# Performance work log

Measured on AMD Instinct MI355X. Metric: run time of the kernel, lower is better.

Reference implementation:

```python
import jax, jax.numpy as jnp
import numpy as np

N_NODES = 50000
N_GRAPHS = 128
N_FEATS = 128
HIDDEN = 128
FC_HID = 64
N_CLASSES = 10
N_EDGES = 600000


def gcn_conv(x, W, b, src, dst, n):
    # x: [N, Fin] -> [N, Fout]; symmetric-normalized scatter aggregation (PyG GCNConv)
    h = x @ W  # [N, Fout]
    ones = jnp.ones(src.shape[0], dtype=h.dtype)
    deg = jax.ops.segment_sum(ones, dst, num_segments=n)  # in-degree incl. self loops
    dinv = jnp.where(deg > 0, jax.lax.rsqrt(jnp.maximum(deg, 1.0)), 0.0)
    norm = dinv[src] * dinv[dst]  # [E]
    msg = norm[:, None] * h[src]  # gather + scale, [E, Fout]
    out = jax.ops.segment_sum(msg, dst, num_segments=n)  # scatter-add
    return out + b


def setup_inputs() -> dict:
    key = jax.random.key(0)
    ks = jax.random.split(key, 16)
    x = jax.random.normal(ks[0], (N_NODES, N_FEATS), dtype=jnp.float32)
    edge_index = jax.random.randint(ks[1], (2, N_EDGES), 0, N_NODES, dtype=jnp.int64)
    batch = jnp.sort(jax.random.randint(ks[2], (N_NODES,), 0, N_GRAPHS, dtype=jnp.int64))

    def lin(k, fin, fout):
        s = 1.0 / np.sqrt(fin)
        kw, kb = jax.random.split(k)
        W = jax.random.uniform(kw, (fin, fout), jnp.float32, -s, s)
        b = jax.random.uniform(kb, (fout,), jnp.float32, -s, s)
        return W, b

    W1, b1 = lin(ks[3], N_FEATS, HIDDEN)
    W2, b2 = lin(ks[4], HIDDEN, HIDDEN)
    W3, b3 = lin(ks[5], HIDDEN, HIDDEN)
    Wf1, bf1 = lin(ks[6], HIDDEN, FC_HID)
    Wf2, bf2 = lin(ks[7], FC_HID, N_CLASSES)
    return {"x": x, "edge_index": edge_index, "batch": batch,
            "W1": W1, "b1": b1, "W2": W2, "b2": b2, "W3": W3, "b3": b3,
            "Wf1": Wf1, "bf1": bf1, "Wf2": Wf2, "bf2": bf2}


def reference(x, edge_index, batch, W1, b1, W2, b2, W3, b3, Wf1, bf1, Wf2, bf2):
    n = x.shape[0]
    # add self loops (PyG GCNConv default)
    loop = jnp.arange(n, dtype=edge_index.dtype)
    src = jnp.concatenate([edge_index[0], loop])
    dst = jnp.concatenate([edge_index[1], loop])

    h = jax.nn.relu(gcn_conv(x, W1, b1, src, dst, n))
    h = jax.nn.relu(gcn_conv(h, W2, b2, src, dst, n))
    h = jax.nn.relu(gcn_conv(h, W3, b3, src, dst, n))

    # global mean pool per graph
    sums = jax.ops.segment_sum(h, batch, num_segments=N_GRAPHS)
    cnts = jax.ops.segment_sum(jnp.ones((n,), h.dtype), batch, num_segments=N_GRAPHS)
    hg = sums / jnp.maximum(cnts, 1.0)[:, None]  # [G, HIDDEN]

    h = jax.nn.relu(hg @ Wf1 + bf1)
    return h @ Wf2 + bf2  # [G, N_CLASSES]
```

## Files before the change

### kernel.cpp

```cpp
#include <hip/hip_runtime.h>

#define NFEAT 128
#define NGRAPHS 128
#define FCH 64
#define NCLS 10
#define ELLW 48

__global__ void ell_fill_kernel(const int* __restrict__ src, const int* __restrict__ dst, int E,
                                int* __restrict__ cursor, int* __restrict__ ell) {
    int i = (blockIdx.x * blockDim.x + threadIdx.x) * 4;
    if (i + 3 < E) {
        int4 s4 = *(const int4*)(src + i);
        int4 d4 = *(const int4*)(dst + i);
        int p;
        p = atomicAdd(&cursor[d4.x], 1); if (p < ELLW) ell[(size_t)d4.x * ELLW + p] = s4.x;
        p = atomicAdd(&cursor[d4.y], 1); if (p < ELLW) ell[(size_t)d4.y * ELLW + p] = s4.y;
        p = atomicAdd(&cursor[d4.z], 1); if (p < ELLW) ell[(size_t)d4.z * ELLW + p] = s4.z;
        p = atomicAdd(&cursor[d4.w], 1); if (p < ELLW) ell[(size_t)d4.w * ELLW + p] = s4.w;
    } else {
        for (int j = i; j < E; ++j) {
            int d = dst[j];
            int p = atomicAdd(&cursor[d], 1);
            if (p < ELLW) ell[(size_t)d * ELLW + p] = src[j];
        }
    }
}

__global__ void dinv_kernel(const int* __restrict__ deg, float* __restrict__ dinv, int N) {
    int i = blockIdx.x * blockDim.x + threadIdx.x;
    if (i < N) dinv[i] = rsqrtf((float)(deg[i] + 1));
}

__global__ __launch_bounds__(256)
void gemm128_kernel(const float* __restrict__ X, const float* __restrict__ W,
                    const float* __restrict__ dinv, float* __restrict__ H, int N) {
    __shared__ float4 Ws4[32 * 32];
    int t = threadIdx.x;
    int tx = t & 15;
    int ty = t >> 4;
    int r0 = blockIdx.x * 128 + ty * 8;

    const float* xr[8];
    bool rowok[8];
    #pragma unroll
    for (int i = 0; i < 8; ++i) {
        rowok[i] = (r0 + i < N);
        xr[i] = X + (size_t)(rowok[i] ? (r0 + i) : 0) * NFEAT;
    }

    float acc[8][8];
    #pragma unroll
    for (int i = 0; i < 8; ++i)
        #pragma unroll
        for (int j = 0; j < 8; ++j) acc[i][j] = 0.f;

    const float4* W4 = (const float4*)W;

    for (int ko = 0; ko < 128; ko += 32) {
        #pragma unroll
        for (int i = 0; i < 4; ++i) Ws4[t + i * 256] = W4[ko * 32 + t + i * 256];
        __syncthreads();

        for (int k = 0; k < 32; k += 4) {
            float xk[8][4];
            #pragma unroll
            for (int i = 0; i < 8; ++i) {
                float4 v = *(const float4*)(xr[i] + ko + k);
                xk[i][0] = v.x; xk[i][1] = v.y; xk[i][2] = v.z; xk[i][3] = v.w;
            }
            #pragma unroll
            for (int kk = 0; kk < 4; ++kk) {
                float4 wa = Ws4[(k + kk) * 32 + tx];
                float4 wb = Ws4[(k + kk) * 32 + 16 + tx];
                float w[8] = {wa.x, wa.y, wa.z, wa.w, wb.x, wb.y, wb.z, wb.w};
                #pragma unroll
                for (int i = 0; i < 8; ++i) {
                    float xv = xk[i][kk];
                    #pragma unroll
                    for (int j = 0; j < 8; ++j) acc[i][j] = fmaf(xv, w[j], acc[i][j]);
                }
            }
        }
        __syncthreads();
    }

    #pragma unroll
    for (int i = 0; i < 8; ++i) {
        if (rowok[i]) {
            float di = dinv[r0 + i];
            float* hp = H + (size_t)(r0 + i) * NFEAT;
            float4 o0 = {di * acc[i][0], di * acc[i][1], di * acc[i][2], di * acc[i][3]};
            float4 o1 = {di * acc[i][4], di * acc[i][5], di * acc[i][6], di * acc[i][7]};
            *(float4*)(hp + tx * 4) = o0;
            *(float4*)(hp + 64 + tx * 4) = o1;
        }
    }
}

__global__ __launch_bounds__(256)
void aggregate_kernel(const float* __restrict__ Hs, const int* __restrict__ deg,
                      const int* __restrict__ ell, const float* __restrict__ dinv,
                      const float* __restrict__ bias, float* __restrict__ out, int N) {
    int node = (blockIdx.x * 256 + threadIdx.x) >> 6;
    int lane = threadIdx.x & 63;
    if (node >= N) return;

    int half = lane >> 5;
    int fl = lane & 31;
    const float4* H4 = (const float4*)Hs;

    float di = dinv[node];
    float4 acc = {0.f, 0.f, 0.f, 0.f};
    if (half == 0) acc = H4[(size_t)node * 32 + fl];

    const int* row = ell + (size_t)node * ELLW;
    int d = deg[node]; if (d > ELLW) d = ELLW;
    int e = 0;

    for (; e + 7 < d; e += 8) {
        int s0 = row[e + half], s1 = row[e + 2 + half];
        int s2 = row[e + 4 + half], s3 = row[e + 6 + half];
        float4 v0 = H4[(size_t)s0 * 32 + fl];
        float4 v1 = H4[(size_t)s1 * 32 + fl];
        float4 v2 = H4[(size_t)s2 * 32 + fl];
        float4 v3 = H4[(size_t)s3 * 32 + fl];
        acc.x += v0.x + v1.x + v2.x + v3.x;
        acc.y += v0.y + v1.y + v2.y + v3.y;
        acc.z += v0.z + v1.z + v2.z + v3.z;
        acc.w += v0.w + v1.w + v2.w + v3.w;
    }
    for (; e + 1 < d; e += 2) {
        int s = row[e + half];
        float4 v = H4[(size_t)s * 32 + fl];
        acc.x += v.x; acc.y += v.y; acc.z += v.z; acc.w += v.w;
    }
    if (e < d && half == 0) {
        int s = row[e];
        float4 v = H4[(size_t)s * 32 + fl];
        acc.x += v.x; acc.y += v.y; acc.z += v.z; acc.w += v.w;
    }

    acc.x += __shfl_down(acc.x, 32, 64);
    acc.y += __shfl_down(acc.y, 32, 64);
    acc.z += __shfl_down(acc.z, 32, 64);
    acc.w += __shfl_down(acc.w, 32, 64);

    if (half == 0) {
        float4 b = ((const float4*)bias)[fl];
        float4 o;
        o.x = fmaxf(fmaf(di, acc.x, b.x), 0.f);
        o.y = fmaxf(fmaf(di, acc.y, b.y), 0.f);
        o.z = fmaxf(fmaf(di, acc.z, b.z), 0.f);
        o.w = fmaxf(fmaf(di, acc.w, b.w), 0.f);
        ((float4*)(out + (size_t)node * NFEAT))[fl] = o;
    }
}

__global__ __launch_bounds__(256)
void poolfc_kernel(const float* __restrict__ H, const int* __restrict__ batch, int N,
                   const float* __restrict__ Wf1, const float* __restrict__ bf1,
                   const float* __restrict__ Wf2, const float* __restrict__ bf2,
                   float* __restrict__ out) {
    int g = blockIdx.x;

    int lo = 0, hi = N;
    while (lo < hi) { int mid = (lo + hi) >> 1; if (batch[mid] < g) lo = mid + 1; else hi = mid; }
    int start = lo;
    hi = N;
    while (lo < hi) { int mid = (lo + hi) >> 1; if (batch[mid] < g + 1) lo = mid + 1; else hi = mid; }
    int end = lo;

    int wave = threadIdx.x >> 6;
    int lane = threadIdx.x & 63;

    float2 acc = {0.f, 0.f};
    for (int i = start + wave; i < end; i += 4) {
        float2 v = ((const float2*)(H + (size_t)i * NFEAT))[lane];
        acc.x += v.x; acc.y += v.y;
    }

    __shared__ float2 part[4][64];
    __shared__ float hg[NFEAT];
    __shared__ float h1[FCH];
    part[wave][lane] = acc;
    __syncthreads();

    if (wave == 0) {
        float2 t0 = part[0][lane], t1 = part[1][lane], t2 = part[2][lane], t3 = part[3][lane];
        float c = fmaxf((float)(end - start), 1.0f);
        hg[lane * 2]     = (t0.x + t1.x + t2.x + t3.x) / c;
        hg[lane * 2 + 1] = (t0.y + t1.y + t2.y + t3.y) / c;
        float a = bf1[lane];
        #pragma unroll 4
        for (int k = 0; k < NFEAT; ++k) a = fmaf(hg[k], Wf1[k * FCH + lane], a);
        h1[lane] = fmaxf(a, 0.f);
        if (lane < NCLS) {
            float o = bf2[lane];
            #pragma unroll
            for (int j = 0; j < FCH; ++j) o = fmaf(h1[j], Wf2[j * NCLS + lane], o);
            out[g * NCLS + lane] = o;
        }
    }
}

extern "C" void kernel_launch(void* const* d_in, const int* in_sizes, int n_in,
                              void* d_out, int out_size, void* d_ws, size_t ws_size,
                              hipStream_t stream) {
    const float* x   = (const float*)d_in[0];
    const int*   ei  = (const int*)d_in[1];
    const int*   bat = (const int*)d_in[2];
    const float* W1  = (const float*)d_in[3];
    const float* b1  = (const float*)d_in[4];
    const float* W2  = (const float*)d_in[5];
    const float* b2  = (const float*)d_in[6];
    const float* W3  = (const float*)d_in[7];
    const float* b3  = (const float*)d_in[8];
    const float* Wf1 = (const float*)d_in[9];
    const float* bf1 = (const float*)d_in[10];
    const float* Wf2 = (const float*)d_in[11];
    const float* bf2 = (const float*)d_in[12];
    float* out = (float*)d_out;

    int N = in_sizes[0] / NFEAT;
    int E = in_sizes[1] / 2;
    const int* src = ei;
    const int* dst = ei + E;

    char* ws = (char*)d_ws;
    size_t off = 0;
    auto align256 = [](size_t v) { return (v + 255) & ~(size_t)255; };

    int* cursor = (int*)(ws + off);
    off = align256(off + (size_t)N * 4);
    int* ell = (int*)(ws + off);
    off = align256(off + (size_t)N * ELLW * 4);
    float* dinv = (float*)(ws + off);
    off = align256(off + (size_t)N * 4);
    float* h0 = (float*)(ws + off);
    off = align256(off + (size_t)N * NFEAT * 4);
    float* h1 = (float*)(ws + off);
    off = align256(off + (size_t)N * NFEAT * 4);

    hipMemsetAsync(cursor, 0, (size_t)N * 4, stream);

    int tpb = 256;
    int e4blocks = ((E + 3) / 4 + tpb - 1) / tpb;
    int nblocks = (N + tpb - 1) / tpb;

    ell_fill_kernel<<<e4blocks, tpb, 0, stream>>>(src, dst, E, cursor, ell);
    dinv_kernel<<<nblocks, tpb, 0, stream>>>(cursor, dinv, N);

    int gemm_blocks = (N + 127) / 128;
    int agg_blocks = (N + 3) / 4;

    gemm128_kernel<<<gemm_blocks, 256, 0, stream>>>(x, W1, dinv, h0, N);
    aggregate_kernel<<<agg_blocks, 256, 0, stream>>>(h0, cursor, ell, dinv, b1, h1, N);
    gemm128_kernel<<<gemm_blocks, 256, 0, stream>>>(h1, W2, dinv, h0, N);
    aggregate_kernel<<<agg_blocks, 256, 0, stream>>>(h0, cursor, ell, dinv, b2, h1, N);
    gemm128_kernel<<<gemm_blocks, 256, 0, stream>>>(h1, W3, dinv, h0, N);
    aggregate_kernel<<<agg_blocks, 256, 0, stream>>>(h0, cursor, ell, dinv, b3, h1, N);

    poolfc_kernel<<<NGRAPHS, 256, 0, stream>>>(h1, bat, N, Wf1, bf1, Wf2, bf2, out);
}
```

Baseline: 392.1 us.

## Fold dinv into consumers, retile GEMM without LDS, widen pooling blocks

Removes the separate dinv kernel and its buffer by computing rsqrt(deg+1) inline in the GEMM epilogue and in the aggregate kernel. The GEMM is retiled to 64-row blocks with 8x4 outputs per thread and reads W directly from global/L2 instead of staging it in LDS, which drops the barriers and shared memory. The pooling/FC kernel moves from 256 to 1024 threads so each graph's sum runs over 16 waves. The GEMM change trades LDS reuse for more global W traffic and less register reuse per thread.

```diff
diff --git a/kernel.cpp b/kernel.cpp
--- a/kernel.cpp
+++ b/kernel.cpp
@@ -26,19 +26,15 @@
     }
 }
 
-__global__ void dinv_kernel(const int* __restrict__ deg, float* __restrict__ dinv, int N) {
-    int i = blockIdx.x * blockDim.x + threadIdx.x;
-    if (i < N) dinv[i] = rsqrtf((float)(deg[i] + 1));
-}
-
 __global__ __launch_bounds__(256)
 void gemm128_kernel(const float* __restrict__ X, const float* __restrict__ W,
-                    const float* __restrict__ dinv, float* __restrict__ H, int N) {
-    __shared__ float4 Ws4[32 * 32];
+                    const int* __restrict__ deg, float* __restrict__ H, int N) {
     int t = threadIdx.x;
-    int tx = t & 15;
-    int ty = t >> 4;
-    int r0 = blockIdx.x * 128 + ty * 8;
+    int tx = t & 31;
+    int ty = t >> 5;
+    int r0 = blockIdx.x * 64 + ty * 8;
+
+    const float4* W4 = (const float4*)W;
 
     const float* xr[8];
     bool rowok[8];
@@ -48,58 +44,44 @@
         xr[i] = X + (size_t)(rowok[i] ? (r0 + i) : 0) * NFEAT;
     }
 
-    float acc[8][8];
+    float acc[8][4];
     #pragma unroll
     for (int i = 0; i < 8; ++i)
         #pragma unroll
-        for (int j = 0; j < 8; ++j) acc[i][j] = 0.f;
-
-    const float4* W4 = (const float4*)W;
-
-    for (int ko = 0; ko < 128; ko += 32) {
-        #pragma unroll
-        for (int i = 0; i < 4; ++i) Ws4[t + i * 256] = W4[ko * 32 + t + i * 256];
-        __syncthreads();
-
-        for (int k = 0; k < 32; k += 4) {
-            float xk[8][4];
+        for (int j = 0; j < 4; ++j) acc[i][j] = 0.f;
+
+    #pragma unroll 2
+    for (int k0 = 0; k0 < 128; k0 += 4) {
+        float4 xv[8];
+        #pragma unroll
+        for (int i = 0; i < 8; ++i) xv[i] = *(const float4*)(xr[i] + k0);
+        #pragma unroll
+        for (int kk = 0; kk < 4; ++kk) {
+            float4 w4 = W4[(k0 + kk) * 32 + tx];
             #pragma unroll
             for (int i = 0; i < 8; ++i) {
-                float4 v = *(const float4*)(xr[i] + ko + k);
-                xk[i][0] = v.x; xk[i][1] = v.y; xk[i][2] = v.z; xk[i][3] = v.w;
+                float xs = (kk == 0) ? xv[i].x : (kk == 1) ? xv[i].y : (kk == 2) ? xv[i].z : xv[i].w;
+                acc[i][0] = fmaf(xs, w4.x, acc[i][0]);
+                acc[i][1] = fmaf(xs, w4.y, acc[i][1]);
+                acc[i][2] = fmaf(xs, w4.z, acc[i][2]);
+                acc[i][3] = fmaf(xs, w4.w, acc[i][3]);
             }
-            #pragma unroll
-            for (int kk = 0; kk < 4; ++kk) {
-                float4 wa = Ws4[(k + kk) * 32 + tx];
-                float4 wb = Ws4[(k + kk) * 32 + 16 + tx];
-                float w[8] = {wa.x, wa.y, wa.z, wa.w, wb.x, wb.y, wb.z, wb.w};
-                #pragma unroll
-                for (int i = 0; i < 8; ++i) {
-                    float xv = xk[i][kk];
-                    #pragma unroll
-                    for (int j = 0; j < 8; ++j) acc[i][j] = fmaf(xv, w[j], acc[i][j]);
-                }
-            }
-        }
-        __syncthreads();
+        }
     }
 
     #pragma unroll
     for (int i = 0; i < 8; ++i) {
         if (rowok[i]) {
-            float di = dinv[r0 + i];
-            float* hp = H + (size_t)(r0 + i) * NFEAT;
-            float4 o0 = {di * acc[i][0], di * acc[i][1], di * acc[i][2], di * acc[i][3]};
-            float4 o1 = {di * acc[i][4], di * acc[i][5], di * acc[i][6], di * acc[i][7]};
-            *(float4*)(hp + tx * 4) = o0;
-            *(float4*)(hp + 64 + tx * 4) = o1;
+            float di = rsqrtf((float)(deg[r0 + i] + 1));
+            float4 o = {di * acc[i][0], di * acc[i][1], di * acc[i][2], di * acc[i][3]};
+            *(float4*)(H + (size_t)(r0 + i) * NFEAT + tx * 4) = o;
         }
     }
 }
 
 __global__ __launch_bounds__(256)
 void aggregate_kernel(const float* __restrict__ Hs, const int* __restrict__ deg,
-                      const int* __restrict__ ell, const float* __restrict__ dinv,
+                      const int* __restrict__ ell,
                       const float* __restrict__ bias, float* __restrict__ out, int N) {
     int node = (blockIdx.x * 256 + threadIdx.x) >> 6;
     int lane = threadIdx.x & 63;
@@ -109,12 +91,13 @@
     int fl = lane & 31;
     const float4* H4 = (const float4*)Hs;
 
-    float di = dinv[node];
+    int dn = deg[node];
+    float di = rsqrtf((float)(dn + 1));
     float4 acc = {0.f, 0.f, 0.f, 0.f};
     if (half == 0) acc = H4[(size_t)node * 32 + fl];
 
     const int* row = ell + (size_t)node * ELLW;
-    int d = deg[node]; if (d > ELLW) d = ELLW;
+    int d = dn; if (d > ELLW) d = ELLW;
     int e = 0;
 
     for (; e + 7 < d; e += 8) {
@@ -156,7 +139,7 @@
     }
 }
 
-__global__ __launch_bounds__(256)
+__global__ __launch_bounds__(1024)
 void poolfc_kernel(const float* __restrict__ H, const int* __restrict__ batch, int N,
                    const float* __restrict__ Wf1, const float* __restrict__ bf1,
                    const float* __restrict__ Wf2, const float* __restrict__ bf2,
@@ -174,22 +157,24 @@
     int lane = threadIdx.x & 63;
 
     float2 acc = {0.f, 0.f};
-    for (int i = start + wave; i < end; i += 4) {
+    for (int i = start + wave; i < end; i += 16) {
         float2 v = ((const float2*)(H + (size_t)i * NFEAT))[lane];
         acc.x += v.x; acc.y += v.y;
     }
 
-    __shared__ float2 part[4][64];
+    __shared__ float2 part[16][64];
     __shared__ float hg[NFEAT];
     __shared__ float h1[FCH];
     part[wave][lane] = acc;
     __syncthreads();
 
     if (wave == 0) {
-        float2 t0 = part[0][lane], t1 = part[1][lane], t2 = part[2][lane], t3 = part[3][lane];
+        float2 tot = {0.f, 0.f};
+        #pragma unroll
+        for (int w = 0; w < 16; ++w) { tot.x += part[w][lane].x; tot.y += part[w][lane].y; }
         float c = fmaxf((float)(end - start), 1.0f);
-        hg[lane * 2]     = (t0.x + t1.x + t2.x + t3.x) / c;
-        hg[lane * 2 + 1] = (t0.y + t1.y + t2.y + t3.y) / c;
+        hg[lane * 2]     = tot.x / c;
+        hg[lane * 2 + 1] = tot.y / c;
         float a = bf1[lane];
         #pragma unroll 4
         for (int k = 0; k < NFEAT; ++k) a = fmaf(hg[k], Wf1[k * FCH + lane], a);
@@ -234,8 +219,6 @@
     off = align256(off + (size_t)N * 4);
     int* ell = (int*)(ws + off);
     off = align256(off + (size_t)N * ELLW * 4);
-    float* dinv = (float*)(ws + off);
-    off = align256(off + (size_t)N * 4);
     float* h0 = (float*)(ws + off);
     off = align256(off + (size_t)N * NFEAT * 4);
     float* h1 = (float*)(ws + off);
@@ -245,20 +228,18 @@
 
     int tpb = 256;
     int e4blocks = ((E + 3) / 4 + tpb - 1) / tpb;
-    int nblocks = (N + tpb - 1) / tpb;
 
     ell_fill_kernel<<<e4blocks, tpb, 0, stream>>>(src, dst, E, cursor, ell);
-    dinv_kernel<<<nblocks, tpb, 0, stream>>>(cursor, dinv, N);
-
-    int gemm_blocks = (N + 127) / 128;
+
+    int gemm_blocks = (N + 63) / 64;
     int agg_blocks = (N + 3) / 4;
 
-    gemm128_kernel<<<gemm_blocks, 256, 0, stream>>>(x, W1, dinv, h0, N);
-    aggregate_kernel<<<agg_blocks, 256, 0, stream>>>(h0, cursor, ell, dinv, b1, h1, N);
-    gemm128_kernel<<<gemm_blocks, 256, 0, stream>>>(h1, W2, dinv, h0, N);
-    aggregate_kernel<<<agg_blocks, 256, 0, stream>>>(h0, cursor, ell, dinv, b2, h1, N);
-    gemm128_kernel<<<gemm_blocks, 256, 0, stream>>>(h1, W3, dinv, h0, N);
-    aggregate_kernel<<<agg_blocks, 256, 0, stream>>>(h0, cursor, ell, dinv, b3, h1, N);
-
-    poolfc_kernel<<<NGRAPHS, 256, 0, stream>>>(h1, bat, N, Wf1, bf1, Wf2, bf2, out);
-}
+    gemm128_kernel<<<gemm_blocks, 256, 0, stream>>>(x, W1, cursor, h0, N);
+    aggregate_kernel<<<agg_blocks, 256, 0, stream>>>(h0, cursor, ell, b1, h1, N);
+    gemm128_kernel<<<gemm_blocks, 256, 0, stream>>>(h1, W2, cursor, h0, N);
+    aggregate_kernel<<<agg_blocks, 256, 0, stream>>>(h0, cursor, ell, b2, h1, N);
+    gemm128_kernel<<<gemm_blocks, 256, 0, stream>>>(h1, W3, cursor, h0, N);
+    aggregate_kernel<<<agg_blocks, 256, 0, stream>>>(h0, cursor, ell, b3, h1, N);
+
+    poolfc_kernel<<<NGRAPHS, 1024, 0, stream>>>(h1, bat, N, Wf1, bf1, Wf2, bf2, out);
+}
```

Result: slower. 441.0 us (+12.5%).
